# Kernel optimization log

Hardware: AMD Instinct MI355X
Metric: run time of the kernel (lower is better)

Reference implementation:

```python
import jax, jax.numpy as jnp
import numpy as np

N = 512        # n_t (sequence length of observations)
D_IN = 128     # input feature dim
PROJ = 128     # proj_dim
ENC = 128      # enc_dim
H = 4          # num_head
E = PROJ // H  # per-head dim = 32
SCALE = 1.0 / np.float32(np.sqrt(E))


def setup_inputs() -> dict:
    key = jax.random.key(0)
    ks = jax.random.split(key, 14)
    g = lambda k, sh: (jax.random.normal(k, sh, jnp.float32) * 0.05)
    inp = jax.random.normal(ks[0], (N, D_IN), jnp.float32)
    # irregular observation times, sorted ascending
    pos = jnp.sort(jax.random.uniform(ks[1], (N,), jnp.float32) * 100.0)
    # PosEncodingBlock frequency vector f: exp(arange(0,enc,2) * -(ln(10000)/enc))
    f = jnp.exp(jnp.arange(0, ENC, 2, dtype=jnp.float32) * (-(np.log(10000.0) / ENC)))
    return {
        "inp": inp, "pos": pos, "f": f,
        "Wq": g(ks[2], (D_IN, PROJ)), "bq": g(ks[3], (PROJ,)),
        "Wk": g(ks[4], (D_IN, PROJ)), "bk": g(ks[5], (PROJ,)),
        "Wv": g(ks[6], (D_IN, PROJ)), "bv": g(ks[7], (PROJ,)),
        "Wqt": g(ks[8], (D_IN, PROJ)), "bqt": g(ks[9], (PROJ,)),
        "Wt": g(ks[10], (ENC, PROJ)), "bt": g(ks[11], (PROJ,)),
    }


def _heads(x):
    # 'n (h e) -> h n e'
    return x.reshape(N, H, E).transpose(1, 0, 2)


def reference(inp, pos, f, Wq, bq, Wk, bk, Wv, bv, Wqt, bqt, Wt, bt):
    q = _heads(inp @ Wq + bq)   # (h, n, e)
    k = _heads(inp @ Wk + bk)
    v = _heads(inp @ Wv + bv)
    qt = _heads(inp @ Wqt + bqt)

    score = jnp.einsum('hne,hme->hnm', q, k) * SCALE  # (h, n, n)

    # Equivariant relative-time positional encoding: (n, n, ENC)
    rel_time = pos[:, None] - pos[None, :]                    # (n, n)
    angles = rel_time[..., None] * f                          # (n, n, ENC/2)
    # rearrange([sin, cos], 'z t l k -> t l (k z)') interleaves sin/cos per freq
    pos_enc = jnp.stack([jnp.sin(angles), jnp.cos(angles)], axis=-1).reshape(N, N, ENC)

    # time_dense then 'n1 n2 (h e) -> h n1 n2 e'
    t = (pos_enc @ Wt + bt).reshape(N, N, H, E).transpose(2, 0, 1, 3)  # (h, n, n, e)
    # tf.linalg.matvec(t, q_t): bias[h,i,j] = sum_e t[h,i,j,e] * qt[h,i,e]
    score = score + jnp.einsum('hnme,hne->hnm', t, qt) * SCALE

    mask = jnp.tril(jnp.ones((N, N), dtype=bool))
    score = jnp.where(mask, score, -jnp.inf)
    weight = jax.nn.softmax(score, axis=-1)
    weight = jnp.where(mask, weight, 0.0)
    # dropout is identity at inference

    out = jnp.einsum('hnm,hme->hne', weight, v)  # (h, n, e)
    return out.transpose(1, 0, 2).reshape(N, PROJ)  # 'h n e -> n (h e)'
```

## Files before the change

kernel.cpp:

```cpp
#include <hip/hip_runtime.h>
#include <math.h>

namespace {
constexpr int N = 512;
constexpr int DIN = 128;
constexpr int PROJ = 128;
constexpr int H = 4;
constexpr int E = 32;
constexpr int KF = 64;
constexpr int FEAT = E + 2*KF;
constexpr float SCALE = 0.17677669529663687f;
constexpr int TI = 8;
constexpr int JQ = 8;
constexpr int CHUNK = 64;
}

__device__ __forceinline__ float wave_max(float v) {
  #pragma unroll
  for (int o = 32; o > 0; o >>= 1) v = fmaxf(v, __shfl_xor(v, o, 64));
  return v;
}
__device__ __forceinline__ float wave_sum(float v) {
  #pragma unroll
  for (int o = 32; o > 0; o >>= 1) v += __shfl_xor(v, o, 64);
  return v;
}

__global__ __launch_bounds__(256)
void proj_feat_kernel(const float* __restrict__ inp,
                      const float* __restrict__ pos, const float* __restrict__ f,
                      const float* __restrict__ Wq, const float* __restrict__ bq,
                      const float* __restrict__ Wk, const float* __restrict__ bk,
                      const float* __restrict__ Wv, const float* __restrict__ bv,
                      const float* __restrict__ Wqt, const float* __restrict__ bqt,
                      const float* __restrict__ Wt, const float* __restrict__ bt,
                      float* __restrict__ Afeat, float* __restrict__ BTk,
                      float* __restrict__ Vmat, float* __restrict__ Btrig,
                      float* __restrict__ c0)
{
  const int bx = blockIdx.x;
  const int t = threadIdx.x;
  const int c = t & 127;

  if (bx < 384) {
    const int mat = bx >> 7, rowTile = bx & 127;
    const int i0 = rowTile * 4;
    const int half = t >> 7;
    __shared__ float x[4][DIN];
    #pragma unroll
    for (int r = 0; r < 2; ++r) {
      const int id = t + r * 256;
      x[id >> 7][id & 127] = inp[i0 * DIN + id];
    }
    const float* W; const float* bvec;
    switch (mat) {
      case 0:  W = Wq; bvec = bq; break;
      case 1:  W = Wk; bvec = bk; break;
      default: W = Wv; bvec = bv; break;
    }
    __syncthreads();
    const int r0 = half * 2, r1 = r0 + 1;
    float a0 = 0.f, a1 = 0.f;
    #pragma unroll 8
    for (int d = 0; d < DIN; d += 2) {
      const float w0 = W[d * PROJ + c];
      const float w1 = W[(d + 1) * PROJ + c];
      const float2 x0 = *(const float2*)&x[r0][d];
      const float2 x1 = *(const float2*)&x[r1][d];
      a0 += w0 * x0.x + w1 * x0.y;
      a1 += w0 * x1.x + w1 * x1.y;
    }
    const float bb = bvec[c];
    a0 += bb; a1 += bb;
    const int h = c >> 5, e = c & 31;
    const int row0 = i0 + r0, row1 = i0 + r1;
    if (mat == 0) {
      Afeat[(h * N + row0) * FEAT + e] = a0;
      Afeat[(h * N + row1) * FEAT + e] = a1;
    } else if (mat == 1) {
      BTk[(size_t)(h * E + e) * N + row0] = a0;
      BTk[(size_t)(h * E + e) * N + row1] = a1;
    } else {
      Vmat[(h * N + row0) * E + e] = a0;
      Vmat[(h * N + row1) * E + e] = a1;
    }
    return;
  }

  const int i0 = (bx - 384) * 2;
  const int r = t >> 7;
  __shared__ float x[2][DIN];
  __shared__ float qt_l[2][PROJ];
  __shared__ float ss[2][KF], sc[2][KF];
  __shared__ float ul[2][H][PROJ];

  x[r][c] = inp[i0 * DIN + t];
  if (t < 128) {
    const int rr = t >> 6, k = t & 63;
    float s_, c_;
    sincosf(pos[i0 + rr] * f[k], &s_, &c_);
    ss[rr][k] = s_; sc[rr][k] = c_;
  }
  __syncthreads();

  {
    float a = 0.f;
    #pragma unroll 8
    for (int d = 0; d < DIN; d += 2) {
      const float w0 = Wqt[d * PROJ + c];
      const float w1 = Wqt[(d + 1) * PROJ + c];
      const float2 xv = *(const float2*)&x[r][d];
      a += w0 * xv.x + w1 * xv.y;
    }
    qt_l[r][c] = a + bqt[c];
  }
  __syncthreads();

  {
    const int g = t >> 7;
    const float* wrow = &Wt[c * PROJ];
    #pragma unroll
    for (int hh = 2 * g; hh < 2 * g + 2; ++hh) {
      float uA = 0.f, uB = 0.f;
      #pragma unroll
      for (int e4 = 0; e4 < E; e4 += 4) {
        const float4 w = *(const float4*)&wrow[hh * E + e4];
        const float4 qA = *(const float4*)&qt_l[0][hh * E + e4];
        const float4 qB = *(const float4*)&qt_l[1][hh * E + e4];
        uA += w.x * qA.x + w.y * qA.y + w.z * qA.z + w.w * qA.w;
        uB += w.x * qB.x + w.y * qB.y + w.z * qB.z + w.w * qB.w;
      }
      ul[0][hh][c] = uA;
      ul[1][hh][c] = uB;
    }
  }
  if (t < 8) {
    const int rr = t & 1, hh = t >> 1;
    float acc = 0.f;
    for (int e2 = 0; e2 < E; ++e2) acc += bt[hh * E + e2] * qt_l[rr][hh * E + e2];
    c0[hh * N + i0 + rr] = acc;
  }
  __syncthreads();

  {
    const int k = t & 63, hh = t >> 6;
    #pragma unroll
    for (int rr = 0; rr < 2; ++rr) {
      const float u0 = ul[rr][hh][2 * k], u1 = ul[rr][hh][2 * k + 1];
      const float s_ = ss[rr][k], c_ = sc[rr][k];
      Afeat[(hh * N + i0 + rr) * FEAT + E + k]      =  u0 * s_ + u1 * c_;
      Afeat[(hh * N + i0 + rr) * FEAT + E + KF + k] = -u0 * c_ + u1 * s_;
      if (hh == 0) {
        Btrig[k * N + i0 + rr]        = c_;
        Btrig[(KF + k) * N + i0 + rr] = s_;
      }
    }
  }
}

__global__ __launch_bounds__(256)
void attn_partial(const float* __restrict__ Afeat, const float* __restrict__ BTk,
                  const float* __restrict__ Btrig, const float* __restrict__ Vmat,
                  const float* __restrict__ c0,
                  float* __restrict__ Po, float* __restrict__ Pm,
                  float* __restrict__ Ps)
{
  const int b = blockIdx.x, h = blockIdx.y, q = blockIdx.z;
  const int i0 = b * TI, jbase = q * CHUNK;
  if (jbase > i0) return;
  const int t = threadIdx.x;
  const int lane = t & 63;
  const int rh = __builtin_amdgcn_readfirstlane(t >> 6);
  const int j = jbase + lane;

  __shared__ float pT[CHUNK][12];
  __shared__ float obuf[16][TI][32];

  const float* A0 = Afeat + (size_t)(h * N + i0 + rh * 2) * FEAT;
  const float* A1 = A0 + FEAT;
  const float cc0 = c0[h * N + i0 + rh * 2];
  const float cc1 = c0[h * N + i0 + rh * 2 + 1];

  float acc0 = 0.f, acc1 = 0.f;
  {
    const float* Bp = BTk + (size_t)h * E * N + j;
    #pragma unroll
    for (int d = 0; d < E; d += 4) {
      const float b0 = Bp[(size_t)(d + 0) * N];
      const float b1 = Bp[(size_t)(d + 1) * N];
      const float b2 = Bp[(size_t)(d + 2) * N];
      const float b3 = Bp[(size_t)(d + 3) * N];
      const float4 a0 = *(const float4*)&A0[d];
      const float4 a1 = *(const float4*)&A1[d];
      acc0 += a0.x * b0 + a0.y * b1 + a0.z * b2 + a0.w * b3;
      acc1 += a1.x * b0 + a1.y * b1 + a1.z * b2 + a1.w * b3;
    }
  }
  {
    const float* Bp = Btrig + j;
    #pragma unroll 8
    for (int d = 0; d < 2 * KF; d += 4) {
      const float b0 = Bp[(size_t)(d + 0) * N];
      const float b1 = Bp[(size_t)(d + 1) * N];
      const float b2 = Bp[(size_t)(d + 2) * N];
      const float b3 = Bp[(size_t)(d + 3) * N];
      const float4 a0 = *(const float4*)&A0[E + d];
      const float4 a1 = *(const float4*)&A1[E + d];
      acc0 += a0.x * b0 + a0.y * b1 + a0.z * b2 + a0.w * b3;
      acc1 += a1.x * b0 + a1.y * b1 + a1.z * b2 + a1.w * b3;
    }
  }

  const int i_0 = i0 + rh * 2, i_1 = i_0 + 1;
  const float s0 = (j <= i_0) ? (acc0 + cc0) * SCALE : -INFINITY;
  const float s1 = (j <= i_1) ? (acc1 + cc1) * SCALE : -INFINITY;

  const float m0 = wave_max(s0);
  const float m1 = wave_max(s1);
  const float p0 = __expf(s0 - m0);
  const float p1 = __expf(s1 - m1);
  const float sum0 = wave_sum(p0);
  const float sum1 = wave_sum(p1);

  *(float2*)&pT[lane][rh * 2] = make_float2(p0, p1);
  if (lane == 0) {
    const int base = (h * N + i_0) * JQ + q;
    Pm[base]      = m0; Ps[base]      = sum0;
    Pm[base + JQ] = m1; Ps[base + JQ] = sum1;
  }
  __syncthreads();

  const int e2 = (t & 15) * 2, gg = t >> 4;
  float2 o[TI];
  #pragma unroll
  for (int r = 0; r < TI; ++r) o[r] = make_float2(0.f, 0.f);
  const float* Vh = Vmat + ((size_t)h * N + jbase) * E + e2;
  #pragma unroll
  for (int it = 0; it < CHUNK / 16; ++it) {
    const int jl = gg + 16 * it;
    const float2 vv = *(const float2*)&Vh[jl * E];
    const float4 pa = *(const float4*)&pT[jl][0];
    const float4 pb = *(const float4*)&pT[jl][4];
    o[0].x += pa.x * vv.x; o[0].y += pa.x * vv.y;
    o[1].x += pa.y * vv.x; o[1].y += pa.y * vv.y;
    o[2].x += pa.z * vv.x; o[2].y += pa.z * vv.y;
    o[3].x += pa.w * vv.x; o[3].y += pa.w * vv.y;
    o[4].x += pb.x * vv.x; o[4].y += pb.x * vv.y;
    o[5].x += pb.y * vv.x; o[5].y += pb.y * vv.y;
    o[6].x += pb.z * vv.x; o[6].y += pb.z * vv.y;
    o[7].x += pb.w * vv.x; o[7].y += pb.w * vv.y;
  }
  #pragma unroll
  for (int r = 0; r < TI; ++r) *(float2*)&obuf[gg][r][e2] = o[r];
  __syncthreads();
  {
    const int r = t >> 5, e = t & 31;
    float tot = 0.f;
    #pragma unroll
    for (int g2 = 0; g2 < 16; ++g2) tot += obuf[g2][r][e];
    Po[((size_t)(h * N + i0 + r) * JQ + q) * E + e] = tot;
  }
}

__global__ __launch_bounds__(256)
void attn_combine(const float* __restrict__ Po, const float* __restrict__ Pm,
                  const float* __restrict__ Ps, float* __restrict__ out)
{
  const int gid = blockIdx.x * 256 + threadIdx.x;
  const int task = gid >> 5, e = gid & 31;
  const int h = task >> 9, i = task & (N - 1);
  const int nq = (i >> 6) + 1;
  float m = -INFINITY;
  for (int qq = 0; qq < nq; ++qq) m = fmaxf(m, Pm[task * JQ + qq]);
  float s = 0.f, o = 0.f;
  for (int qq = 0; qq < nq; ++qq) {
    const float w = __expf(Pm[task * JQ + qq] - m);
    s += Ps[task * JQ + qq] * w;
    o += Po[(size_t)(task * JQ + qq) * E + e] * w;
  }
  out[i * PROJ + h * E + e] = o / s;
}

extern "C" void kernel_launch(void* const* d_in, const int* in_sizes, int n_in,
                              void* d_out, int out_size, void* d_ws, size_t ws_size,
                              hipStream_t stream) {
  const float* inp = (const float*)d_in[0];
  const float* pos = (const float*)d_in[1];
  const float* f   = (const float*)d_in[2];
  const float* Wq  = (const float*)d_in[3];
  const float* bq  = (const float*)d_in[4];
  const float* Wk  = (const float*)d_in[5];
  const float* bk  = (const float*)d_in[6];
  const float* Wv  = (const float*)d_in[7];
  const float* bv  = (const float*)d_in[8];
  const float* Wqt = (const float*)d_in[9];
  const float* bqt = (const float*)d_in[10];
  const float* Wt  = (const float*)d_in[11];
  const float* bt  = (const float*)d_in[12];
  float* out = (float*)d_out;

  float* ws    = (float*)d_ws;
  float* Afeat = ws;
  float* BTk   = Afeat + H * N * FEAT;
  float* Btrig = BTk + (size_t)H * E * N;
  float* Vmat  = Btrig + 2 * KF * N;
  float* c0    = Vmat + H * N * E;
  float* Po    = c0 + H * N;
  float* Pm    = Po + (size_t)H * N * JQ * E;
  float* Ps    = Pm + H * N * JQ;

  proj_feat_kernel<<<640, 256, 0, stream>>>(inp, pos, f, Wq, bq, Wk, bk, Wv, bv,
                                            Wqt, bqt, Wt, bt,
                                            Afeat, BTk, Vmat, Btrig, c0);
  attn_partial<<<dim3(N / TI, H, JQ), 256, 0, stream>>>(Afeat, BTk, Btrig, Vmat,
                                                        c0, Po, Pm, Ps);
  attn_combine<<<H * N * E / 256, 256, 0, stream>>>(Po, Pm, Ps, out);
}
```

Measured before the change: 28.20 us.

## Drop softmax max-subtraction, compact triangular grid, pre-transpose Wt for coalescing

The attention partial kernel now launches only the lower-triangular (row block, key chunk) pairs, decoded from a flat index, instead of launching a full grid whose blocks exit early. It also removes the running-max step of the softmax, so exponentials are taken directly and the combine kernel just sums the partials, which eliminates the wave max reductions and the Pm buffer. A separate small kernel transposes Wt so the time-dense projection reads weights with coalesced accesses. Removing the max shift risks overflow if scores grow large, and the transpose adds an extra launch.

```diff
diff --git a/kernel.cpp b/kernel.cpp
--- a/kernel.cpp
+++ b/kernel.cpp
@@ -15,15 +15,17 @@
 constexpr int CHUNK = 64;
 }
 
-__device__ __forceinline__ float wave_max(float v) {
-  #pragma unroll
-  for (int o = 32; o > 0; o >>= 1) v = fmaxf(v, __shfl_xor(v, o, 64));
-  return v;
-}
 __device__ __forceinline__ float wave_sum(float v) {
   #pragma unroll
   for (int o = 32; o > 0; o >>= 1) v += __shfl_xor(v, o, 64);
   return v;
+}
+
+__global__ __launch_bounds__(256)
+void transpose_wt(const float* __restrict__ Wt, float* __restrict__ WtT) {
+  const int idx = blockIdx.x * 256 + threadIdx.x;
+  const int c = idx >> 7, p = idx & 127;
+  WtT[p * PROJ + c] = Wt[idx];
 }
 
 __global__ __launch_bounds__(256)
@@ -33,7 +35,7 @@
                       const float* __restrict__ Wk, const float* __restrict__ bk,
                       const float* __restrict__ Wv, const float* __restrict__ bv,
                       const float* __restrict__ Wqt, const float* __restrict__ bqt,
-                      const float* __restrict__ Wt, const float* __restrict__ bt,
+                      const float* __restrict__ WtT, const float* __restrict__ bt,
                       float* __restrict__ Afeat, float* __restrict__ BTk,
                       float* __restrict__ Vmat, float* __restrict__ Btrig,
                       float* __restrict__ c0)
@@ -118,17 +120,14 @@
 
   {
     const int g = t >> 7;
-    const float* wrow = &Wt[c * PROJ];
     #pragma unroll
     for (int hh = 2 * g; hh < 2 * g + 2; ++hh) {
       float uA = 0.f, uB = 0.f;
-      #pragma unroll
-      for (int e4 = 0; e4 < E; e4 += 4) {
-        const float4 w = *(const float4*)&wrow[hh * E + e4];
-        const float4 qA = *(const float4*)&qt_l[0][hh * E + e4];
-        const float4 qB = *(const float4*)&qt_l[1][hh * E + e4];
-        uA += w.x * qA.x + w.y * qA.y + w.z * qA.z + w.w * qA.w;
-        uB += w.x * qB.x + w.y * qB.y + w.z * qB.z + w.w * qB.w;
+      #pragma unroll 8
+      for (int e = 0; e < E; ++e) {
+        const float w = WtT[(hh * E + e) * PROJ + c];
+        uA += w * qt_l[0][hh * E + e];
+        uB += w * qt_l[1][hh * E + e];
       }
       ul[0][hh][c] = uA;
       ul[1][hh][c] = uB;
@@ -162,12 +161,19 @@
 void attn_partial(const float* __restrict__ Afeat, const float* __restrict__ BTk,
                   const float* __restrict__ Btrig, const float* __restrict__ Vmat,
                   const float* __restrict__ c0,
-                  float* __restrict__ Po, float* __restrict__ Pm,
-                  float* __restrict__ Ps)
+                  float* __restrict__ Po, float* __restrict__ Ps)
 {
-  const int b = blockIdx.x, h = blockIdx.y, q = blockIdx.z;
+  const int fidx = blockIdx.x, h = blockIdx.y;
+  int g = (int)((sqrtf((float)fidx + 1.0f) - 1.0f) * 0.5f);
+  while (4 * (g + 1) * (g + 2) <= fidx) ++g;
+  while (4 * g * (g + 1) > fidx) --g;
+  const int rem = fidx - 4 * g * (g + 1);
+  const int nc = g + 1;
+  const int lb = rem / nc;
+  const int q = rem - lb * nc;
+  const int b = 8 * g + lb;
   const int i0 = b * TI, jbase = q * CHUNK;
-  if (jbase > i0) return;
+
   const int t = threadIdx.x;
   const int lane = t & 63;
   const int rh = __builtin_amdgcn_readfirstlane(t >> 6);
@@ -212,21 +218,16 @@
   }
 
   const int i_0 = i0 + rh * 2, i_1 = i_0 + 1;
-  const float s0 = (j <= i_0) ? (acc0 + cc0) * SCALE : -INFINITY;
-  const float s1 = (j <= i_1) ? (acc1 + cc1) * SCALE : -INFINITY;
-
-  const float m0 = wave_max(s0);
-  const float m1 = wave_max(s1);
-  const float p0 = __expf(s0 - m0);
-  const float p1 = __expf(s1 - m1);
+  const float p0 = (j <= i_0) ? __expf((acc0 + cc0) * SCALE) : 0.f;
+  const float p1 = (j <= i_1) ? __expf((acc1 + cc1) * SCALE) : 0.f;
   const float sum0 = wave_sum(p0);
   const float sum1 = wave_sum(p1);
 
   *(float2*)&pT[lane][rh * 2] = make_float2(p0, p1);
   if (lane == 0) {
     const int base = (h * N + i_0) * JQ + q;
-    Pm[base]      = m0; Ps[base]      = sum0;
-    Pm[base + JQ] = m1; Ps[base + JQ] = sum1;
+    Ps[base]      = sum0;
+    Ps[base + JQ] = sum1;
   }
   __syncthreads();
 
@@ -263,20 +264,17 @@
 }
 
 __global__ __launch_bounds__(256)
-void attn_combine(const float* __restrict__ Po, const float* __restrict__ Pm,
-                  const float* __restrict__ Ps, float* __restrict__ out)
+void attn_combine(const float* __restrict__ Po, const float* __restrict__ Ps,
+                  float* __restrict__ out)
 {
   const int gid = blockIdx.x * 256 + threadIdx.x;
   const int task = gid >> 5, e = gid & 31;
   const int h = task >> 9, i = task & (N - 1);
   const int nq = (i >> 6) + 1;
-  float m = -INFINITY;
-  for (int qq = 0; qq < nq; ++qq) m = fmaxf(m, Pm[task * JQ + qq]);
   float s = 0.f, o = 0.f;
   for (int qq = 0; qq < nq; ++qq) {
-    const float w = __expf(Pm[task * JQ + qq] - m);
-    s += Ps[task * JQ + qq] * w;
-    o += Po[(size_t)(task * JQ + qq) * E + e] * w;
+    s += Ps[task * JQ + qq];
+    o += Po[(size_t)(task * JQ + qq) * E + e];
   }
   out[i * PROJ + h * E + e] = o / s;
 }
@@ -300,19 +298,20 @@
   float* out = (float*)d_out;
 
   float* ws    = (float*)d_ws;
-  float* Afeat = ws;
+  float* WtT   = ws;
+  float* Afeat = WtT + PROJ * PROJ;
   float* BTk   = Afeat + H * N * FEAT;
   float* Btrig = BTk + (size_t)H * E * N;
   float* Vmat  = Btrig + 2 * KF * N;
   float* c0    = Vmat + H * N * E;
   float* Po    = c0 + H * N;
-  float* Pm    = Po + (size_t)H * N * JQ * E;
-  float* Ps    = Pm + H * N * JQ;
-
+  float* Ps    = Po + (size_t)H * N * JQ * E;
+
+  transpose_wt<<<PROJ * PROJ / 256, 256, 0, stream>>>(Wt, WtT);
   proj_feat_kernel<<<640, 256, 0, stream>>>(inp, pos, f, Wq, bq, Wk, bk, Wv, bv,
-                                            Wqt, bqt, Wt, bt,
+                                            Wqt, bqt, WtT, bt,
                                             Afeat, BTk, Vmat, Btrig, c0);
-  attn_partial<<<dim3(N / TI, H, JQ), 256, 0, stream>>>(Afeat, BTk, Btrig, Vmat,
-                                                        c0, Po, Pm, Ps);
-  attn_combine<<<H * N * E / 256, 256, 0, stream>>>(Po, Pm, Ps, out);
-}
+  attn_partial<<<dim3(288, H), 256, 0, stream>>>(Afeat, BTk, Btrig, Vmat,
+                                                 c0, Po, Ps);
+  attn_combine<<<H * N * E / 256, 256, 0, stream>>>(Po, Ps, out);
+}
```

Measured after the change: 33.80 us. +19.9%, slower.
